# Kernel optimization log

Measured on AMD Instinct MI355X. Metric: run time of the kernel, lower is better.

## Reference

```python
import jax, jax.numpy as jnp
import numpy as np

EMBED = 1024
HEADS = 16
HEAD_DIM = EMBED // HEADS


def setup_inputs() -> dict:
    key = jax.random.key(0)
    k1, k2, k3 = jax.random.split(key, 3)
    hidden_states = jax.random.normal(k1, (2, 2048, EMBED), dtype=jnp.float32)
    # Conv1D weights are stored (nx, nf): y = x @ W + b
    c_attn_w = jax.random.normal(k2, (EMBED, 3 * EMBED), dtype=jnp.float32) * 0.02
    c_attn_b = jnp.zeros((3 * EMBED,), dtype=jnp.float32)
    c_proj_w = jax.random.normal(k3, (EMBED, EMBED), dtype=jnp.float32) * 0.02
    c_proj_b = jnp.zeros((EMBED,), dtype=jnp.float32)
    return {
        "hidden_states": hidden_states,
        "c_attn_w": c_attn_w,
        "c_attn_b": c_attn_b,
        "c_proj_w": c_proj_w,
        "c_proj_b": c_proj_b,
    }


def reference(hidden_states, c_attn_w, c_attn_b, c_proj_w, c_proj_b):
    B, S, E = hidden_states.shape
    H, D = HEADS, HEAD_DIM
    fused = hidden_states @ c_attn_w + c_attn_b  # [B,S,3E]
    q, k, v = jnp.split(fused, 3, axis=-1)
    # split heads -> [B,H,S,D]
    q = q.reshape(B, S, H, D).transpose(0, 2, 1, 3)
    k = k.reshape(B, S, H, D).transpose(0, 2, 1, 3)
    v = v.reshape(B, S, H, D).transpose(0, 2, 1, 3)
    scores = jnp.einsum("bhqd,bhkd->bhqk", q, k) / jnp.sqrt(jnp.float32(D))
    probs = jax.nn.softmax(scores, axis=-1)  # NOTE: no causal mask in source
    attn = jnp.einsum("bhqk,bhkd->bhqd", probs, v)
    out = attn.transpose(0, 2, 1, 3).reshape(B, S, E)
    return out @ c_proj_w + c_proj_b
```

## Files before the change

kernel.cpp:

```cpp
#include <hip/hip_runtime.h>
#include <hip/hip_bf16.h>
#include <cstdint>
#include <cstddef>

#define E_ 1024
#define H_ 16
#define D_ 64
#define B_ 2
#define S_ 2048
#define T_ 4096
#define NQ_ 3072

typedef __bf16 bf16_t;
typedef bf16_t bf16x8 __attribute__((ext_vector_type(8)));
typedef float f32x4 __attribute__((ext_vector_type(4)));

static __device__ __forceinline__ unsigned short f2bf(float f) {
    __hip_bfloat16 h = __float2bfloat16(f);
    return __builtin_bit_cast(unsigned short, h);
}
static __device__ __forceinline__ unsigned pack2(float a, float b) {
    return (unsigned)f2bf(a) | ((unsigned)f2bf(b) << 16);
}
static __device__ __forceinline__ unsigned cvt_pk(float a, float b) {
    unsigned r;
    asm("v_cvt_pk_bf16_f32 %0, %1, %2" : "=v"(r) : "v"(a), "v"(b));
    return r;
}
static __device__ __forceinline__ bf16x8 ld_frag(const unsigned short* p) {
    uint4 u = *reinterpret_cast<const uint4*>(p);
    return __builtin_bit_cast(bf16x8, u);
}
static __device__ __forceinline__ void cp16(unsigned short* lds, const unsigned short* g) {
    __builtin_amdgcn_global_load_lds(
        (const __attribute__((address_space(1))) unsigned int*)g,
        (__attribute__((address_space(3))) unsigned int*)lds, 16, 0, 0);
}
static __device__ __forceinline__ f32x4 mfma16(bf16x8 a, bf16x8 b, f32x4 c) {
    return __builtin_amdgcn_mfma_f32_16x16x32_bf16(a, b, c, 0, 0, 0);
}

__global__ __launch_bounds__(256) void k_cvt(const float* __restrict__ in,
                                             unsigned short* __restrict__ out, int n) {
    int i = (blockIdx.x * 256 + threadIdx.x) * 4;
    if (i < n) {
        float4 v = *reinterpret_cast<const float4*>(in + i);
        uint2 o;
        o.x = pack2(v.x, v.y);
        o.y = pack2(v.z, v.w);
        *reinterpret_cast<uint2*>(out + i) = o;
    }
}

__global__ __launch_bounds__(256) void k_wt(const float* __restrict__ in,
                                            unsigned short* __restrict__ out, int K, int N) {
    __shared__ float t[32][33];
    int n0 = blockIdx.x * 32, k0 = blockIdx.y * 32;
    int tx = threadIdx.x, ty = threadIdx.y;
    for (int j = 0; j < 4; j++) {
        int r = ty + j * 8;
        t[r][tx] = in[(size_t)(k0 + r) * N + n0 + tx];
    }
    __syncthreads();
    for (int j = 0; j < 4; j++) {
        int r = ty + j * 8;
        out[(size_t)(n0 + r) * K + k0 + tx] = f2bf(t[tx][r]);
    }
}

static __device__ __forceinline__ void gemm_tile_128(
    const unsigned short* __restrict__ A,
    const unsigned short* __restrict__ Bt,
    int Ktot, int m0, int n0,
    unsigned short* As, unsigned short* Bs,
    f32x4 acc[4][4])
{
    const int t = threadIdx.x;
    const int w = t >> 6, lane = t & 63, lr = lane & 15, lq = lane >> 4;
    const int wm = (w >> 1) * 64, wn = (w & 1) * 64;
    for (int mt = 0; mt < 4; mt++)
        for (int nt = 0; nt < 4; nt++)
            acc[mt][nt] = (f32x4){0.f, 0.f, 0.f, 0.f};

    for (int kt = 0; kt < Ktot; kt += 32) {
        __syncthreads();
        for (int i = 0; i < 2; i++) {
            int c = t + i * 256;
            int row = c >> 2, kp = (c & 3) * 8;
            cp16(&As[c * 8], &A[(size_t)(m0 + row) * Ktot + kt + kp]);
        }
        for (int i = 0; i < 2; i++) {
            int c = t + i * 256;
            int row = c >> 2, kp = (c & 3) * 8;
            cp16(&Bs[c * 8], &Bt[(size_t)(n0 + row) * Ktot + kt + kp]);
        }
        __syncthreads();
        bf16x8 af[4], bfr[4];
        for (int mt = 0; mt < 4; mt++) af[mt]  = ld_frag(&As[(wm + mt * 16 + lr) * 32 + lq * 8]);
        for (int nt = 0; nt < 4; nt++) bfr[nt] = ld_frag(&Bs[(wn + nt * 16 + lr) * 32 + lq * 8]);
        for (int mt = 0; mt < 4; mt++)
            for (int nt = 0; nt < 4; nt++)
                acc[mt][nt] = mfma16(af[mt], bfr[nt], acc[mt][nt]);
    }
}

__global__ __launch_bounds__(256) void k_qkv(
    const unsigned short* __restrict__ Ab, const unsigned short* __restrict__ Wt,
    const float* __restrict__ bias,
    unsigned short* __restrict__ Qb, unsigned short* __restrict__ Kb,
    unsigned short* __restrict__ Vb)
{
    __shared__ __attribute__((aligned(16))) unsigned short As[128 * 32];
    __shared__ __attribute__((aligned(16))) unsigned short Bs[128 * 32];
    f32x4 acc[4][4];
    int m0 = blockIdx.x * 128, n0 = blockIdx.y * 128;
    gemm_tile_128(Ab, Wt, E_, m0, n0, As, Bs, acc);

    int t = threadIdx.x, w = t >> 6, lane = t & 63, lr = lane & 15, lq = lane >> 4;
    int wm = (w >> 1) * 64, wn = (w & 1) * 64;
    int sector = (n0 >> 10);
    for (int nt = 0; nt < 4; nt++) {
        int n = n0 + wn + nt * 16 + lr;
        float bv = bias[n];
        int nn = n & 1023, h = nn >> 6, d = nn & 63;
        for (int mt = 0; mt < 4; mt++) {
            for (int i = 0; i < 4; i++) {
                int tok = m0 + wm + mt * 16 + lq * 4 + i;
                int b = tok >> 11, s = tok & 2047;
                float v = acc[mt][nt][i] + bv;
                if (sector == 0) {
                    Qb[(((size_t)(b * H_ + h) * S_ + s) << 6) + d] = f2bf(v * 0.18033688f);
                } else if (sector == 1) {
                    Kb[(((size_t)(b * H_ + h) * S_ + s) << 6) + d] = f2bf(v);
                } else {
                    Vb[(((size_t)(b * H_ + h) * D_ + d) << 11) + s] = f2bf(v);
                }
            }
        }
    }
}

__global__ __launch_bounds__(256) void k_attn(
    const unsigned short* __restrict__ Qb, const unsigned short* __restrict__ Kb,
    const unsigned short* __restrict__ Vb, unsigned short* __restrict__ Ob)
{
    __shared__ __attribute__((aligned(16))) unsigned short Ks[2][64 * 64];
    __shared__ __attribute__((aligned(16))) unsigned short Vt[2][64 * 64];
    __shared__ __attribute__((aligned(16))) unsigned short Ps[4][32 * 64];

    const int t = threadIdx.x, w = t >> 6, lane = t & 63, lr = lane & 15, lq = lane >> 4;
    const int h = blockIdx.y, b = blockIdx.z;
    const size_t head = ((size_t)(b * H_ + h)) * (S_ * D_);
    const unsigned short* Qh = Qb + head;
    const unsigned short* Kh = Kb + head;
    const unsigned short* Vh = Vb + head;
    const int q0 = blockIdx.x * 128 + w * 16;
    const int swz = lr & 7;

    bf16x8 qa[2][2];
    for (int qh = 0; qh < 2; qh++)
        for (int kk = 0; kk < 2; kk++)
            qa[qh][kk] = ld_frag(&Qh[(size_t)(q0 + qh * 64 + lr) * 64 + kk * 32 + lq * 8]);

    f32x4 o[2][4];
    for (int qh = 0; qh < 2; qh++)
        for (int i = 0; i < 4; i++) o[qh][i] = (f32x4){0.f, 0.f, 0.f, 0.f};
    float lsum[2] = {0.f, 0.f};
    unsigned short* Pw = Ps[w];

    auto stage = [&](int bb, int kt) {
        for (int i = 0; i < 2; i++) {
            int c = t + i * 256;
            int row = c >> 3, sp = c & 7, seg = sp ^ (row & 7);
            cp16(&Ks[bb][c * 8], &Kh[(size_t)(kt + row) * 64 + seg * 8]);
        }
        for (int i = 0; i < 2; i++) {
            int c = t + i * 256;
            int d = c >> 3, sp = c & 7, seg = sp ^ (d & 7);
            cp16(&Vt[bb][c * 8], &Vh[(size_t)d * S_ + kt + seg * 8]);
        }
    };

    stage(0, 0);
    asm volatile("s_waitcnt vmcnt(0)" ::: "memory");
    __syncthreads();

    int cur = 0;
#pragma unroll 2
    for (int kt = 0; kt < S_; kt += 64) {
        if (kt + 64 < S_) stage(cur ^ 1, kt + 64);

        const unsigned short* Kc = Ks[cur];
        const unsigned short* Vc = Vt[cur];

        for (int tau = 0; tau < 4; tau++) {
            bf16x8 kf0 = ld_frag(&Kc[(tau * 16 + lr) * 64 + ((0 + lq) ^ swz) * 8]);
            bf16x8 kf1 = ld_frag(&Kc[(tau * 16 + lr) * 64 + ((4 + lq) ^ swz) * 8]);
            for (int qh = 0; qh < 2; qh++) {
                f32x4 z = (f32x4){0.f, 0.f, 0.f, 0.f};
                __builtin_amdgcn_s_setprio(1);
                z = mfma16(kf0, qa[qh][0], z);
                z = mfma16(kf1, qa[qh][1], z);
                __builtin_amdgcn_s_setprio(0);
                float e0 = __builtin_amdgcn_exp2f(z[0]);
                float e1 = __builtin_amdgcn_exp2f(z[1]);
                float e2 = __builtin_amdgcn_exp2f(z[2]);
                float e3 = __builtin_amdgcn_exp2f(z[3]);
                lsum[qh] += (e0 + e1) + (e2 + e3);
                uint2 pk;
                pk.x = cvt_pk(e0, e1);
                pk.y = cvt_pk(e2, e3);
                int seg = (tau * 2 + (lq >> 1)) ^ swz;
                *reinterpret_cast<uint2*>(&Pw[(qh * 16 + lr) * 64 + seg * 8 + (lq & 1) * 4]) = pk;
            }
        }
        for (int kk = 0; kk < 2; kk++) {
            bf16x8 pf0 = ld_frag(&Pw[(lr) * 64 + ((kk * 4 + lq) ^ swz) * 8]);
            bf16x8 pf1 = ld_frag(&Pw[(16 + lr) * 64 + ((kk * 4 + lq) ^ swz) * 8]);
            __builtin_amdgcn_s_setprio(1);
            for (int t2 = 0; t2 < 4; t2++) {
                bf16x8 vf = ld_frag(&Vc[(t2 * 16 + lr) * 64 + ((kk * 4 + lq) ^ swz) * 8]);
                o[0][t2] = mfma16(vf, pf0, o[0][t2]);
                o[1][t2] = mfma16(vf, pf1, o[1][t2]);
            }
            __builtin_amdgcn_s_setprio(0);
        }

        asm volatile("s_waitcnt vmcnt(0)" ::: "memory");
        __syncthreads();
        cur ^= 1;
    }

    for (int qh = 0; qh < 2; qh++) {
        float ls = lsum[qh];
        ls += __shfl_xor(ls, 16, 64);
        ls += __shfl_xor(ls, 32, 64);
        float inv = 1.0f / ls;

        int s = q0 + qh * 64 + lr;
        size_t rowoff = ((size_t)(b * S_ + s)) * E_ + h * 64;
        for (int t2 = 0; t2 < 4; t2++) {
            uint2 pk;
            pk.x = cvt_pk(o[qh][t2][0] * inv, o[qh][t2][1] * inv);
            pk.y = cvt_pk(o[qh][t2][2] * inv, o[qh][t2][3] * inv);
            *reinterpret_cast<uint2*>(&Ob[rowoff + t2 * 16 + lq * 4]) = pk;
        }
    }
}

__global__ __launch_bounds__(256) void k_proj(
    const unsigned short* __restrict__ Ab, const unsigned short* __restrict__ Wt,
    const float* __restrict__ bias, float* __restrict__ out)
{
    __shared__ __attribute__((aligned(16))) unsigned short As[128 * 32];
    __shared__ __attribute__((aligned(16))) unsigned short Bs[128 * 32];
    f32x4 acc[4][4];
    int m0 = blockIdx.x * 128, n0 = blockIdx.y * 128;
    gemm_tile_128(Ab, Wt, E_, m0, n0, As, Bs, acc);

    int t = threadIdx.x, w = t >> 6, lane = t & 63, lr = lane & 15, lq = lane >> 4;
    int wm = (w >> 1) * 64, wn = (w & 1) * 64;
    for (int nt = 0; nt < 4; nt++) {
        int n = n0 + wn + nt * 16 + lr;
        float bv = bias[n];
        for (int mt = 0; mt < 4; mt++)
            for (int i = 0; i < 4; i++) {
                int tok = m0 + wm + mt * 16 + lq * 4 + i;
                out[(size_t)tok * E_ + n] = acc[mt][nt][i] + bv;
            }
    }
}

extern "C" void kernel_launch(void* const* d_in, const int* in_sizes, int n_in,
                              void* d_out, int out_size, void* d_ws, size_t ws_size,
                              hipStream_t stream) {
    const float* hs = (const float*)d_in[0];
    const float* w1 = (const float*)d_in[1];
    const float* b1 = (const float*)d_in[2];
    const float* w2 = (const float*)d_in[3];
    const float* b2 = (const float*)d_in[4];
    float* out = (float*)d_out;

    char* ws = (char*)d_ws;
    unsigned short* hb  = (unsigned short*)(ws);
    unsigned short* w1t = (unsigned short*)(ws + (size_t)( 8 << 20));
    unsigned short* w2t = (unsigned short*)(ws + (size_t)(14 << 20));
    unsigned short* Qb  = (unsigned short*)(ws + (size_t)(16 << 20));
    unsigned short* Kb  = (unsigned short*)(ws + (size_t)(24 << 20));
    unsigned short* Vb  = (unsigned short*)(ws + (size_t)(32 << 20));
    unsigned short* Ao  = (unsigned short*)(ws + (size_t)(40 << 20));

    k_cvt<<<dim3(T_ * E_ / 1024), dim3(256), 0, stream>>>(hs, hb, T_ * E_);
    k_wt<<<dim3(NQ_ / 32, E_ / 32), dim3(32, 8), 0, stream>>>(w1, w1t, E_, NQ_);
    k_wt<<<dim3(E_ / 32, E_ / 32), dim3(32, 8), 0, stream>>>(w2, w2t, E_, E_);
    k_qkv<<<dim3(T_ / 128, NQ_ / 128), dim3(256), 0, stream>>>(hb, w1t, b1, Qb, Kb, Vb);
    k_attn<<<dim3(S_ / 128, H_, B_), dim3(256), 0, stream>>>(Qb, Kb, Vb, Ao);
    k_proj<<<dim3(T_ / 128, E_ / 128), dim3(256), 0, stream>>>(Ao, w2t, b2, out);
}
```

Baseline: 194.3 us.

## Double attention KV tile to 128 keys and narrow projection GEMM tiles to 128x64

The attention kernel now stages 128 keys of K and V per loop iteration instead of 64. This halves the number of barriers and global-load waits across the key sequence, at the cost of twice the LDS for the K/V buffers. The output projection kernel moves from 128x128 to 128x64 tiles with an inline GEMM loop, doubling the block count (256 to 512) so more of the GPU's compute units are occupied. The inline loop has no double buffering, so load latency is exposed more.

```diff
diff --git a/kernel.cpp b/kernel.cpp
--- a/kernel.cpp
+++ b/kernel.cpp
@@ -144,8 +144,8 @@
     const unsigned short* __restrict__ Qb, const unsigned short* __restrict__ Kb,
     const unsigned short* __restrict__ Vb, unsigned short* __restrict__ Ob)
 {
-    __shared__ __attribute__((aligned(16))) unsigned short Ks[2][64 * 64];
-    __shared__ __attribute__((aligned(16))) unsigned short Vt[2][64 * 64];
+    __shared__ __attribute__((aligned(16))) unsigned short Ks[2][128 * 64];
+    __shared__ __attribute__((aligned(16))) unsigned short Vt[2][64 * 128];
     __shared__ __attribute__((aligned(16))) unsigned short Ps[4][32 * 64];
 
     const int t = threadIdx.x, w = t >> 6, lane = t & 63, lr = lane & 15, lq = lane >> 4;
@@ -169,14 +169,14 @@
     unsigned short* Pw = Ps[w];
 
     auto stage = [&](int bb, int kt) {
-        for (int i = 0; i < 2; i++) {
-            int c = t + i * 256;
-            int row = c >> 3, sp = c & 7, seg = sp ^ (row & 7);
-            cp16(&Ks[bb][c * 8], &Kh[(size_t)(kt + row) * 64 + seg * 8]);
-        }
-        for (int i = 0; i < 2; i++) {
-            int c = t + i * 256;
-            int d = c >> 3, sp = c & 7, seg = sp ^ (d & 7);
+        for (int i = 0; i < 4; i++) {
+            int c = t + i * 256;
+            int row = c >> 3, sp = c & 7;
+            cp16(&Ks[bb][c * 8], &Kh[(size_t)(kt + row) * 64 + (sp ^ (row & 7)) * 8]);
+        }
+        for (int i = 0; i < 4; i++) {
+            int c = t + i * 256;
+            int d = c >> 4, sp = c & 15, seg = (sp & 8) | ((sp & 7) ^ (d & 7));
             cp16(&Vt[bb][c * 8], &Vh[(size_t)d * S_ + kt + seg * 8]);
         }
     };
@@ -187,43 +187,48 @@
 
     int cur = 0;
 #pragma unroll 2
-    for (int kt = 0; kt < S_; kt += 64) {
-        if (kt + 64 < S_) stage(cur ^ 1, kt + 64);
+    for (int kt = 0; kt < S_; kt += 128) {
+        if (kt + 128 < S_) stage(cur ^ 1, kt + 128);
 
         const unsigned short* Kc = Ks[cur];
         const unsigned short* Vc = Vt[cur];
 
-        for (int tau = 0; tau < 4; tau++) {
-            bf16x8 kf0 = ld_frag(&Kc[(tau * 16 + lr) * 64 + ((0 + lq) ^ swz) * 8]);
-            bf16x8 kf1 = ld_frag(&Kc[(tau * 16 + lr) * 64 + ((4 + lq) ^ swz) * 8]);
-            for (int qh = 0; qh < 2; qh++) {
-                f32x4 z = (f32x4){0.f, 0.f, 0.f, 0.f};
+#pragma unroll
+        for (int ss = 0; ss < 2; ss++) {
+            for (int tau = 0; tau < 4; tau++) {
+                int krow = ss * 64 + tau * 16 + lr;
+                bf16x8 kf0 = ld_frag(&Kc[krow * 64 + ((0 + lq) ^ swz) * 8]);
+                bf16x8 kf1 = ld_frag(&Kc[krow * 64 + ((4 + lq) ^ swz) * 8]);
+                for (int qh = 0; qh < 2; qh++) {
+                    f32x4 z = (f32x4){0.f, 0.f, 0.f, 0.f};
+                    __builtin_amdgcn_s_setprio(1);
+                    z = mfma16(kf0, qa[qh][0], z);
+                    z = mfma16(kf1, qa[qh][1], z);
+                    __builtin_amdgcn_s_setprio(0);
+                    float e0 = __builtin_amdgcn_exp2f(z[0]);
+                    float e1 = __builtin_amdgcn_exp2f(z[1]);
+                    float e2 = __builtin_amdgcn_exp2f(z[2]);
+                    float e3 = __builtin_amdgcn_exp2f(z[3]);
+                    lsum[qh] += (e0 + e1) + (e2 + e3);
+                    uint2 pk;
+                    pk.x = cvt_pk(e0, e1);
+                    pk.y = cvt_pk(e2, e3);
+                    int seg = (tau * 2 + (lq >> 1)) ^ swz;
+                    *reinterpret_cast<uint2*>(&Pw[(qh * 16 + lr) * 64 + seg * 8 + (lq & 1) * 4]) = pk;
+                }
+            }
+            for (int kk = 0; kk < 2; kk++) {
+                bf16x8 pf0 = ld_frag(&Pw[(lr) * 64 + ((kk * 4 + lq) ^ swz) * 8]);
+                bf16x8 pf1 = ld_frag(&Pw[(16 + lr) * 64 + ((kk * 4 + lq) ^ swz) * 8]);
                 __builtin_amdgcn_s_setprio(1);
-                z = mfma16(kf0, qa[qh][0], z);
-                z = mfma16(kf1, qa[qh][1], z);
+                for (int t2 = 0; t2 < 4; t2++) {
+                    int vrow = t2 * 16 + lr;
+                    bf16x8 vf = ld_frag(&Vc[vrow * 128 + ((ss * 8) | ((kk * 4 + lq) ^ swz)) * 8]);
+                    o[0][t2] = mfma16(vf, pf0, o[0][t2]);
+                    o[1][t2] = mfma16(vf, pf1, o[1][t2]);
+                }
                 __builtin_amdgcn_s_setprio(0);
-                float e0 = __builtin_amdgcn_exp2f(z[0]);
-                float e1 = __builtin_amdgcn_exp2f(z[1]);
-                float e2 = __builtin_amdgcn_exp2f(z[2]);
-                float e3 = __builtin_amdgcn_exp2f(z[3]);
-                lsum[qh] += (e0 + e1) + (e2 + e3);
-                uint2 pk;
-                pk.x = cvt_pk(e0, e1);
-                pk.y = cvt_pk(e2, e3);
-                int seg = (tau * 2 + (lq >> 1)) ^ swz;
-                *reinterpret_cast<uint2*>(&Pw[(qh * 16 + lr) * 64 + seg * 8 + (lq & 1) * 4]) = pk;
             }
-        }
-        for (int kk = 0; kk < 2; kk++) {
-            bf16x8 pf0 = ld_frag(&Pw[(lr) * 64 + ((kk * 4 + lq) ^ swz) * 8]);
-            bf16x8 pf1 = ld_frag(&Pw[(16 + lr) * 64 + ((kk * 4 + lq) ^ swz) * 8]);
-            __builtin_amdgcn_s_setprio(1);
-            for (int t2 = 0; t2 < 4; t2++) {
-                bf16x8 vf = ld_frag(&Vc[(t2 * 16 + lr) * 64 + ((kk * 4 + lq) ^ swz) * 8]);
-                o[0][t2] = mfma16(vf, pf0, o[0][t2]);
-                o[1][t2] = mfma16(vf, pf1, o[1][t2]);
-            }
-            __builtin_amdgcn_s_setprio(0);
         }
 
         asm volatile("s_waitcnt vmcnt(0)" ::: "memory");
@@ -253,14 +258,39 @@
     const float* __restrict__ bias, float* __restrict__ out)
 {
     __shared__ __attribute__((aligned(16))) unsigned short As[128 * 32];
-    __shared__ __attribute__((aligned(16))) unsigned short Bs[128 * 32];
-    f32x4 acc[4][4];
-    int m0 = blockIdx.x * 128, n0 = blockIdx.y * 128;
-    gemm_tile_128(Ab, Wt, E_, m0, n0, As, Bs, acc);
-
-    int t = threadIdx.x, w = t >> 6, lane = t & 63, lr = lane & 15, lq = lane >> 4;
-    int wm = (w >> 1) * 64, wn = (w & 1) * 64;
-    for (int nt = 0; nt < 4; nt++) {
+    __shared__ __attribute__((aligned(16))) unsigned short Bs[64 * 32];
+    const int t = threadIdx.x;
+    const int w = t >> 6, lane = t & 63, lr = lane & 15, lq = lane >> 4;
+    const int wm = (w >> 1) * 64, wn = (w & 1) * 32;
+    const int m0 = blockIdx.x * 128, n0 = blockIdx.y * 64;
+
+    f32x4 acc[4][2];
+    for (int mt = 0; mt < 4; mt++)
+        for (int nt = 0; nt < 2; nt++)
+            acc[mt][nt] = (f32x4){0.f, 0.f, 0.f, 0.f};
+
+    for (int kt = 0; kt < E_; kt += 32) {
+        __syncthreads();
+        for (int i = 0; i < 2; i++) {
+            int c = t + i * 256;
+            int row = c >> 2, kp = (c & 3) * 8;
+            cp16(&As[c * 8], &Ab[(size_t)(m0 + row) * E_ + kt + kp]);
+        }
+        {
+            int c = t;
+            int row = c >> 2, kp = (c & 3) * 8;
+            cp16(&Bs[c * 8], &Wt[(size_t)(n0 + row) * E_ + kt + kp]);
+        }
+        __syncthreads();
+        bf16x8 af[4], bfr[2];
+        for (int mt = 0; mt < 4; mt++) af[mt]  = ld_frag(&As[(wm + mt * 16 + lr) * 32 + lq * 8]);
+        for (int nt = 0; nt < 2; nt++) bfr[nt] = ld_frag(&Bs[(wn + nt * 16 + lr) * 32 + lq * 8]);
+        for (int mt = 0; mt < 4; mt++)
+            for (int nt = 0; nt < 2; nt++)
+                acc[mt][nt] = mfma16(af[mt], bfr[nt], acc[mt][nt]);
+    }
+
+    for (int nt = 0; nt < 2; nt++) {
         int n = n0 + wn + nt * 16 + lr;
         float bv = bias[n];
         for (int mt = 0; mt < 4; mt++)
@@ -295,5 +325,5 @@
     k_wt<<<dim3(E_ / 32, E_ / 32), dim3(32, 8), 0, stream>>>(w2, w2t, E_, E_);
     k_qkv<<<dim3(T_ / 128, NQ_ / 128), dim3(256), 0, stream>>>(hb, w1t, b1, Qb, Kb, Vb);
     k_attn<<<dim3(S_ / 128, H_, B_), dim3(256), 0, stream>>>(Qb, Kb, Vb, Ao);
-    k_proj<<<dim3(T_ / 128, E_ / 128), dim3(256), 0, stream>>>(Ao, w2t, b2, out);
-}
+    k_proj<<<dim3(T_ / 128, E_ / 64), dim3(256), 0, stream>>>(Ao, w2t, b2, out);
+}
```

Result: no change. 190.9 us (-1.7%).
